# Kernel tuning notes

Measured on AMD Instinct MI355X. Metric: run time of the kernel, lower is better.

The kernel has to match this reference:

```python
import jax, jax.numpy as jnp
import numpy as np

DIM = 768

def setup_inputs() -> dict:
    key = jax.random.key(0)
    k1, k2, k3, k4, k5 = jax.random.split(key, 5)
    B, S, D = 16, 1024, DIM
    x = jax.random.normal(k1, (B, S, D), dtype=jnp.float32)
    # torch Linear weights: W has shape [out, in], y = x @ W.T + b
    w_qkv = jax.random.normal(k2, (3 * D, D), dtype=jnp.float32) * (D ** -0.5)
    b_qkv = jax.random.normal(k3, (3 * D,), dtype=jnp.float32) * 0.01
    w_out = jax.random.normal(k4, (D, D), dtype=jnp.float32) * (D ** -0.5)
    b_out = jax.random.normal(k5, (D,), dtype=jnp.float32) * 0.01
    return {"x": x, "w_qkv": w_qkv, "b_qkv": b_qkv, "w_out": w_out, "b_out": b_out}

def reference(x, w_qkv, b_qkv, w_out, b_out):
    D = x.shape[-1]
    qkv = jnp.einsum('bsd,ed->bse', x, w_qkv) + b_qkv  # [B,S,3D]
    q, k, v = jnp.split(qkv, 3, axis=-1)
    scale = D ** -0.5
    att = jnp.einsum('bqd,bkd->bqk', q, k) * scale  # [B,S,S]
    att = jax.nn.softmax(att, axis=-1)
    # dropout (p=0.1) is identity in eval mode
    out = jnp.einsum('bqk,bkd->bqd', att, v)
    return jnp.einsum('bsd,ed->bse', out, w_out) + b_out
```

## Files before the change

kernel.cpp:

```cpp
#include <hip/hip_runtime.h>
#include <hip/hip_bf16.h>
#include <math.h>

typedef __attribute__((ext_vector_type(8))) short bf16x8;
typedef __attribute__((ext_vector_type(4))) float f32x4;

__device__ __forceinline__ unsigned short f2bf_rne(float f) {
    union { float f; unsigned u; } x; x.f = f;
    unsigned r = x.u + 0x7FFFu + ((x.u >> 16) & 1u);
    return (unsigned short)(r >> 16);
}

__device__ __forceinline__ void store4(unsigned short* p, float v0, float v1, float v2, float v3) {
    ushort4 o; o.x = f2bf_rne(v0); o.y = f2bf_rne(v1); o.z = f2bf_rne(v2); o.w = f2bf_rne(v3);
    *(ushort4*)p = o;
}
__device__ __forceinline__ void store4(float* p, float v0, float v1, float v2, float v3) {
    float4 o; o.x = v0; o.y = v1; o.z = v2; o.w = v3;
    *(float4*)p = o;
}

__device__ __forceinline__ void async_copy16(const void* g, void* l) {
    __builtin_amdgcn_global_load_lds(
        (const __attribute__((address_space(1))) void*)g,
        (__attribute__((address_space(3))) void*)l, 16, 0, 0);
}

__device__ __forceinline__ void gemm_core128(
    unsigned short* shA, unsigned short* shB,
    const unsigned short* __restrict__ A, int lda,
    const unsigned short* __restrict__ B, int ldb,
    long long tileM, long long tileN, int K,
    int t, int wm, int wn, int quad, int l16, f32x4 (&acc)[4][4])
{
    for (int k0 = 0; k0 < K; k0 += 64) {
        __syncthreads();
#pragma unroll
        for (int p = 0; p < 4; ++p) {
            const int g   = p * 256 + t;
            const int row = g >> 3;
            const int kg  = (g & 7) ^ (row & 7);
            async_copy16(A + (tileM + row) * (long long)lda + k0 + kg * 8, &shA[g << 3]);
            async_copy16(B + (tileN + row) * (long long)ldb + k0 + kg * 8, &shB[g << 3]);
        }
        __syncthreads();

#pragma unroll 1
        for (int h = 0; h < 2; ++h) {
            bf16x8 af[4], bfr[4];
#pragma unroll
            for (int mi = 0; mi < 4; ++mi) {
                const int row = wm + mi * 16 + l16;
                const int kg  = ((h << 2) | quad) ^ (row & 7);
                af[mi] = *(const bf16x8*)(&shA[row * 64 + kg * 8]);
            }
#pragma unroll
            for (int ni = 0; ni < 4; ++ni) {
                const int row = wn + ni * 16 + l16;
                const int kg  = ((h << 2) | quad) ^ (row & 7);
                bfr[ni] = *(const bf16x8*)(&shB[row * 64 + kg * 8]);
            }
#pragma unroll
            for (int mi = 0; mi < 4; ++mi)
#pragma unroll
                for (int ni = 0; ni < 4; ++ni)
                    acc[mi][ni] = __builtin_amdgcn_mfma_f32_16x16x32_bf16(
                        bfr[ni], af[mi], acc[mi][ni], 0, 0, 0);
        }
    }
}

__global__ __launch_bounds__(256) void prep(
    const float* __restrict__ w_qkv, const float* __restrict__ b_qkv,
    const float* __restrict__ w_out, const float* __restrict__ b_out,
    unsigned short* __restrict__ wqT, unsigned short* __restrict__ wkT,
    unsigned short* __restrict__ wvT, unsigned short* __restrict__ wob,
    float* __restrict__ v2f, float* __restrict__ bpp)
{
    const int blk = blockIdx.x;
    const int t   = threadIdx.x;
    if (blk < 432) {
        __shared__ float sh[64][65];
        __shared__ float pv[4][64];
        const int m  = blk / 144;
        const int r  = blk % 144;
        const int ty = r / 12;
        const int tx = r % 12;
        const float* W = w_qkv + (long long)m * 768 * 768;
        unsigned short* WT = (m == 0) ? wqT : (m == 1) ? wkT : wvT;
        const int il = t & 63;
        const int ob = t >> 6;
        float acc = 0.f;
#pragma unroll
        for (int it = 0; it < 16; ++it) {
            const int ol = ob + it * 4;
            float w = W[(long long)(ty * 64 + ol) * 768 + tx * 64 + il];
            sh[ol][il] = w;
            if (m == 1) acc += w * b_qkv[ty * 64 + ol];
        }
        __syncthreads();
#pragma unroll
        for (int it = 0; it < 16; ++it) {
            const int il2 = ob + it * 4;
            WT[(long long)(tx * 64 + il2) * 768 + ty * 64 + il] = f2bf_rne(sh[il][il2]);
        }
        if (m == 1) {
            pv[ob][il] = acc;
            __syncthreads();
            if (t < 64)
                atomicAdd(&v2f[tx * 64 + t], pv[0][t] + pv[1][t] + pv[2][t] + pv[3][t]);
        }
    } else if (blk < 624) {
        const int d = (blk - 432) * 4 + (t >> 6);
        const int l = t & 63;
        float s = 0.f;
        for (int o = l; o < 768; o += 64)
            s += w_out[(long long)d * 768 + o] * b_qkv[1536 + o];
        for (int off = 1; off < 64; off <<= 1) s += __shfl_xor(s, off);
        if (l == 0) bpp[d] = b_out[d] + s;
    } else {
        const int j = (blk - 624) * 256 + t;
        float4 v = ((const float4*)w_out)[j];
        ushort4 o;
        o.x = f2bf_rne(v.x); o.y = f2bf_rne(v.y);
        o.z = f2bf_rne(v.z); o.w = f2bf_rne(v.w);
        ((ushort4*)wob)[j] = o;
    }
}

__global__ __launch_bounds__(256) void wgemm_cvt(
    const unsigned short* __restrict__ wkT, const unsigned short* __restrict__ wqT,
    const unsigned short* __restrict__ wob, const unsigned short* __restrict__ wvT,
    unsigned short* __restrict__ B2,
    const float* __restrict__ x, unsigned short* __restrict__ xb,
    const float* __restrict__ v2f, float* __restrict__ wf)
{
    const int t = threadIdx.x;
    if (blockIdx.x < 72) {
        __shared__ unsigned short shA[8192];
        __shared__ unsigned short shB[8192];
        const int lane = t & 63;
        const int wave = t >> 6;
        const int wm   = (wave & 1) * 64;
        const int wn   = (wave >> 1) * 64;
        const int quad = lane >> 4;
        const int l16  = lane & 15;
        const int z  = blockIdx.x / 36;
        const int r  = blockIdx.x % 36;
        const long long tileM = (long long)(r / 6) * 128;
        const long long tileN = (long long)(r % 6) * 128;
        const unsigned short* A  = z ? wob : wkT;
        const unsigned short* Bp = z ? wvT : wqT;
        unsigned short* C = B2 + (long long)z * 768 * 768;

        f32x4 acc[4][4];
#pragma unroll
        for (int i = 0; i < 4; ++i)
#pragma unroll
            for (int j = 0; j < 4; ++j)
#pragma unroll
                for (int rr = 0; rr < 4; ++rr) acc[i][j][rr] = 0.0f;

        gemm_core128(shA, shB, A, 768, Bp, 768, tileM, tileN, 768,
                     t, wm, wn, quad, l16, acc);

#pragma unroll
        for (int mi = 0; mi < 4; ++mi) {
            const long long gm = tileM + wm + mi * 16 + l16;
#pragma unroll
            for (int ni = 0; ni < 4; ++ni) {
                const long long gn0 = tileN + wn + ni * 16 + quad * 4;
                const f32x4 a = acc[mi][ni];
                store4(C + gm * 768 + gn0, a[0], a[1], a[2], a[3]);
            }
        }
    } else {
        const int wave = t >> 6;
        const int lane = t & 63;
        const long long row = (long long)(blockIdx.x - 72) * 4 + wave;
        const float4* xr = (const float4*)x + row * 192;
        ushort4* xbr = (ushort4*)xb + row * 192;
        const float4* v2 = (const float4*)v2f;
        float w = 0.f;
#pragma unroll
        for (int j = 0; j < 3; ++j) {
            const int c = j * 64 + lane;
            float4 v = xr[c];
            ushort4 o;
            o.x = f2bf_rne(v.x); o.y = f2bf_rne(v.y);
            o.z = f2bf_rne(v.z); o.w = f2bf_rne(v.w);
            xbr[c] = o;
            float4 b = v2[c];
            w += v.x * b.x + v.y * b.y + v.z * b.z + v.w * b.w;
        }
#pragma unroll
        for (int off = 1; off < 64; off <<= 1) w += __shfl_xor(w, off);
        if (lane == 0) wf[row] = w;
    }
}

template <typename OutT, bool DO_EXP, bool DO_RSCALE, bool DO_VT>
__global__ __launch_bounds__(256) void gemm_nt_bf16(
    const unsigned short* __restrict__ A, int lda, long long strideA,
    const unsigned short* __restrict__ B, int ldb, long long strideB,
    OutT* __restrict__ C, int ldc, long long strideC,
    const float* __restrict__ bias, float scale, int K,
    float* __restrict__ rowsum, const float* __restrict__ rscale,
    unsigned short* __restrict__ vtp, const float* __restrict__ wf)
{
    __shared__ unsigned short shA[8448];
    __shared__ unsigned short shB[8448];

    const int t    = threadIdx.x;
    const int lane = t & 63;
    const int wave = t >> 6;
    const int wm   = (wave & 1) * 64;
    const int wn   = (wave >> 1) * 64;
    const int quad = lane >> 4;
    const int l16  = lane & 15;

    const int gx = gridDim.x, gy = gridDim.y;
    const int nwg = gx * gy * gridDim.z;
    const int orig = blockIdx.x + gx * (blockIdx.y + gy * blockIdx.z);
    const int id  = (orig & 7) * (nwg >> 3) + (orig >> 3);
    const int bx  = id % gx;
    const int rem = id / gx;
    const int by  = rem % gy;
    const int bz  = rem / gy;

    const long long batch = bz;
    A += batch * strideA;
    B += batch * strideB;
    C += batch * strideC;

    const long long tileM = (long long)by * 128;
    const long long tileN = (long long)bx * 128;
    const long long rowsPerBatch = (long long)gy * 128;

    f32x4 acc[4][4];
#pragma unroll
    for (int i = 0; i < 4; ++i)
#pragma unroll
        for (int j = 0; j < 4; ++j)
#pragma unroll
            for (int r = 0; r < 4; ++r) acc[i][j][r] = 0.0f;

    gemm_core128(shA, shB, A, lda, B, ldb, tileM, tileN, K, t, wm, wn, quad, l16, acc);

    const bool vt_block = DO_VT && (tileN >= 768) && (tileN < 1536);
    if (vt_block) __syncthreads();
    unsigned short* const shd = (wn == 0) ? shA : shB;

    float wkv[4][4];
    if (DO_EXP) {
        const float* wfb = wf + batch * rowsPerBatch;
#pragma unroll
        for (int ni = 0; ni < 4; ++ni) {
            const long long gn0 = tileN + wn + ni * 16 + quad * 4;
            float4 t4 = *(const float4*)&wfb[gn0];
            wkv[ni][0] = t4.x; wkv[ni][1] = t4.y; wkv[ni][2] = t4.z; wkv[ni][3] = t4.w;
        }
    }
#pragma unroll
    for (int mi = 0; mi < 4; ++mi) {
        const long long gm = tileM + wm + mi * 16 + l16;
        float w = scale;
        if (DO_RSCALE) w = scale / rscale[batch * rowsPerBatch + gm];
        float rsum = 0.0f;
#pragma unroll
        for (int ni = 0; ni < 4; ++ni) {
            const long long gn0 = tileN + wn + ni * 16 + quad * 4;
            float b0 = 0.f, b1 = 0.f, b2 = 0.f, b3 = 0.f;
            if (bias) {
                float4 bv = *(const float4*)&bias[gn0];
                b0 = bv.x; b1 = bv.y; b2 = bv.z; b3 = bv.w;
            }
            const f32x4 a = acc[mi][ni];
            float v0, v1, v2, v3;
            if (DO_EXP) {
                v0 = __expf((a[0] + wkv[ni][0]) * scale);
                v1 = __expf((a[1] + wkv[ni][1]) * scale);
                v2 = __expf((a[2] + wkv[ni][2]) * scale);
                v3 = __expf((a[3] + wkv[ni][3]) * scale);
                rsum += (v0 + v1) + (v2 + v3);
            } else {
                v0 = a[0] * w + b0; v1 = a[1] * w + b1;
                v2 = a[2] * w + b2; v3 = a[3] * w + b3;
            }
            if (vt_block) {
                const int dl = ni * 16 + quad * 4;
                const int kl = wm + mi * 16 + l16;
                shd[(dl + 0) * 132 + kl] = f2bf_rne(v0);
                shd[(dl + 1) * 132 + kl] = f2bf_rne(v1);
                shd[(dl + 2) * 132 + kl] = f2bf_rne(v2);
                shd[(dl + 3) * 132 + kl] = f2bf_rne(v3);
            } else {
                store4(C + gm * (long long)ldc + gn0, v0, v1, v2, v3);
            }
        }
        if (DO_EXP) {
            rsum += __shfl_xor(rsum, 16);
            rsum += __shfl_xor(rsum, 32);
            if (quad == 0)
                atomicAdd(&rowsum[batch * rowsPerBatch + gm], rsum);
        }
    }
    if (vt_block) {
        __syncthreads();
        const long long bvt  = tileM >> 10;
        const long long kin0 = tileM & 1023;
        const int dr = t >> 1;
        const int hf = t & 1;
        const unsigned short* src = (dr < 64) ? &shA[dr * 132] : &shB[(dr - 64) * 132];
        unsigned short* dst = vtp + (bvt * 768 + (tileN - 768) + dr) * 1024 + kin0 + hf * 64;
        src += hf * 64;
#pragma unroll
        for (int j = 0; j < 16; ++j)
            *(uint2*)(dst + j * 4) = *(const uint2*)(src + j * 4);
    }
}

extern "C" void kernel_launch(void* const* d_in, const int* in_sizes, int n_in,
                              void* d_out, int out_size, void* d_ws, size_t ws_size,
                              hipStream_t stream) {
    (void)in_sizes; (void)n_in; (void)out_size; (void)ws_size;

    const float* x     = (const float*)d_in[0];
    const float* w_qkv = (const float*)d_in[1];
    const float* b_qkv = (const float*)d_in[2];
    const float* w_out = (const float*)d_in[3];
    const float* b_out = (const float*)d_in[4];
    float* out = (float*)d_out;

    const int B = 16, S = 1024, D = 768;
    const long long MS = (long long)B * S;
    const int NB2 = 1536;

    unsigned short* xb  = (unsigned short*)d_ws;
    unsigned short* wob = xb  + MS * D;
    unsigned short* wqT = wob + (long long)D * D;
    unsigned short* wkT = wqT + (long long)D * D;
    unsigned short* wvT = wkT + (long long)D * D;
    unsigned short* B2  = wvT + (long long)D * D;
    unsigned short* xm  = B2  + (long long)NB2 * D;
    unsigned short* vwt = xm  + MS * NB2;
    unsigned short* att = vwt + (long long)B * D * S;
    float* rsum = (float*)(att + (long long)B * S * S);
    float* v2f  = rsum + MS;
    float* bpp  = v2f + D;
    float* wf   = bpp + D;

    hipMemsetAsync(rsum, 0, (size_t)(MS + D) * sizeof(float), stream);

    prep<<<1200, 256, 0, stream>>>(w_qkv, b_qkv, w_out, b_out,
                                   wqT, wkT, wvT, wob, v2f, bpp);

    wgemm_cvt<<<4168, 256, 0, stream>>>(wkT, wqT, wob, wvT, B2, x, xb, v2f, wf);

    gemm_nt_bf16<unsigned short, false, false, true><<<dim3(NB2 / 128, (int)(MS / 128), 1), 256, 0, stream>>>(
        xb, D, 0, B2, D, 0, xm, NB2, 0, nullptr, 1.0f, D, nullptr, nullptr, vwt, nullptr);

    const float scale = 0.03608439182435162f;
    gemm_nt_bf16<unsigned short, true, false, false><<<dim3(S / 128, S / 128, B), 256, 0, stream>>>(
        xm, NB2, (long long)S * NB2,
        xb, D,   (long long)S * D,
        att, S,  (long long)S * S, nullptr, scale, D, rsum, nullptr, nullptr, wf);

    gemm_nt_bf16<float, false, true, false><<<dim3(D / 128, S / 128, B), 256, 0, stream>>>(
        att, S, (long long)S * S,
        vwt, S, (long long)D * S,
        out, D, (long long)S * D, bpp, 1.0f, S, nullptr, rsum, nullptr, nullptr);
}
```

Baseline: 259.8 us.

## Replace atomic row-sum accumulation with partial-sum slots and fold softmax scale into weights

Row sums of the exponentiated scores are now written to 16 per-column-tile partial slots instead of being accumulated with atomicAdd. The final GEMM adds those slots up, which removes the hipMemsetAsync and the atomic contention. The QK scale is folded into the precomputed Wk^T Wq product and the wf vector, so the exp epilogue loses one multiply per element. The k-bias vector is now computed in dedicated prep blocks without atomics, and xm gets a tighter stride of 768 instead of 1536. The cost is extra reads of 16 partials per row in the output GEMM.

```diff
diff --git a/kernel.cpp b/kernel.cpp
--- a/kernel.cpp
+++ b/kernel.cpp
@@ -4,6 +4,8 @@
 
 typedef __attribute__((ext_vector_type(8))) short bf16x8;
 typedef __attribute__((ext_vector_type(4))) float f32x4;
+
+#define SCALE_QK 0.03608439182435162f
 
 __device__ __forceinline__ unsigned short f2bf_rne(float f) {
     union { float f; unsigned u; } x; x.f = f;
@@ -81,7 +83,6 @@
     const int t   = threadIdx.x;
     if (blk < 432) {
         __shared__ float sh[64][65];
-        __shared__ float pv[4][64];
         const int m  = blk / 144;
         const int r  = blk % 144;
         const int ty = r / 12;
@@ -90,25 +91,16 @@
         unsigned short* WT = (m == 0) ? wqT : (m == 1) ? wkT : wvT;
         const int il = t & 63;
         const int ob = t >> 6;
-        float acc = 0.f;
 #pragma unroll
         for (int it = 0; it < 16; ++it) {
             const int ol = ob + it * 4;
-            float w = W[(long long)(ty * 64 + ol) * 768 + tx * 64 + il];
-            sh[ol][il] = w;
-            if (m == 1) acc += w * b_qkv[ty * 64 + ol];
+            sh[ol][il] = W[(long long)(ty * 64 + ol) * 768 + tx * 64 + il];
         }
         __syncthreads();
 #pragma unroll
         for (int it = 0; it < 16; ++it) {
             const int il2 = ob + it * 4;
             WT[(long long)(tx * 64 + il2) * 768 + ty * 64 + il] = f2bf_rne(sh[il][il2]);
-        }
-        if (m == 1) {
-            pv[ob][il] = acc;
-            __syncthreads();
-            if (t < 64)
-                atomicAdd(&v2f[tx * 64 + t], pv[0][t] + pv[1][t] + pv[2][t] + pv[3][t]);
         }
     } else if (blk < 624) {
         const int d = (blk - 432) * 4 + (t >> 6);
@@ -118,8 +110,20 @@
             s += w_out[(long long)d * 768 + o] * b_qkv[1536 + o];
         for (int off = 1; off < 64; off <<= 1) s += __shfl_xor(s, off);
         if (l == 0) bpp[d] = b_out[d] + s;
+    } else if (blk < 636) {
+        __shared__ float pvv[4][64];
+        const int i0   = (blk - 624) * 64;
+        const int il   = t & 63;
+        const int wave = t >> 6;
+        const float* Wk = w_qkv + 768LL * 768;
+        float a = 0.f;
+        for (int o = wave * 192; o < wave * 192 + 192; ++o)
+            a += Wk[(long long)o * 768 + i0 + il] * b_qkv[o];
+        pvv[wave][il] = a;
+        __syncthreads();
+        if (t < 64) v2f[i0 + t] = pvv[0][t] + pvv[1][t] + pvv[2][t] + pvv[3][t];
     } else {
-        const int j = (blk - 624) * 256 + t;
+        const int j = (blk - 636) * 256 + t;
         float4 v = ((const float4*)w_out)[j];
         ushort4 o;
         o.x = f2bf_rne(v.x); o.y = f2bf_rne(v.y);
@@ -152,6 +156,7 @@
         const unsigned short* A  = z ? wob : wkT;
         const unsigned short* Bp = z ? wvT : wqT;
         unsigned short* C = B2 + (long long)z * 768 * 768;
+        const float sc = z ? 1.0f : SCALE_QK;
 
         f32x4 acc[4][4];
 #pragma unroll
@@ -171,7 +176,7 @@
             for (int ni = 0; ni < 4; ++ni) {
                 const long long gn0 = tileN + wn + ni * 16 + quad * 4;
                 const f32x4 a = acc[mi][ni];
-                store4(C + gm * 768 + gn0, a[0], a[1], a[2], a[3]);
+                store4(C + gm * 768 + gn0, a[0] * sc, a[1] * sc, a[2] * sc, a[3] * sc);
             }
         }
     } else {
@@ -195,7 +200,7 @@
         }
 #pragma unroll
         for (int off = 1; off < 64; off <<= 1) w += __shfl_xor(w, off);
-        if (lane == 0) wf[row] = w;
+        if (lane == 0) wf[row] = w * SCALE_QK;
     }
 }
 
@@ -265,7 +270,13 @@
     for (int mi = 0; mi < 4; ++mi) {
         const long long gm = tileM + wm + mi * 16 + l16;
         float w = scale;
-        if (DO_RSCALE) w = scale / rscale[batch * rowsPerBatch + gm];
+        if (DO_RSCALE) {
+            float s = 0.f;
+#pragma unroll
+            for (int j = 0; j < 16; ++j)
+                s += rscale[((long long)j * gridDim.z + batch) * rowsPerBatch + gm];
+            w = scale / s;
+        }
         float rsum = 0.0f;
 #pragma unroll
         for (int ni = 0; ni < 4; ++ni) {
@@ -278,10 +289,10 @@
             const f32x4 a = acc[mi][ni];
             float v0, v1, v2, v3;
             if (DO_EXP) {
-                v0 = __expf((a[0] + wkv[ni][0]) * scale);
-                v1 = __expf((a[1] + wkv[ni][1]) * scale);
-                v2 = __expf((a[2] + wkv[ni][2]) * scale);
-                v3 = __expf((a[3] + wkv[ni][3]) * scale);
+                v0 = __expf(a[0] + wkv[ni][0]);
+                v1 = __expf(a[1] + wkv[ni][1]);
+                v2 = __expf(a[2] + wkv[ni][2]);
+                v3 = __expf(a[3] + wkv[ni][3]);
                 rsum += (v0 + v1) + (v2 + v3);
             } else {
                 v0 = a[0] * w + b0; v1 = a[1] * w + b1;
@@ -301,8 +312,10 @@
         if (DO_EXP) {
             rsum += __shfl_xor(rsum, 16);
             rsum += __shfl_xor(rsum, 32);
-            if (quad == 0)
-                atomicAdd(&rowsum[batch * rowsPerBatch + gm], rsum);
+            if (quad == 0) {
+                const long long slot = (long long)(bx * 2 + (wn >> 6));
+                rowsum[(slot * gridDim.z + batch) * rowsPerBatch + gm] = rsum;
+            }
         }
     }
     if (vt_block) {
@@ -343,31 +356,28 @@
     unsigned short* wvT = wkT + (long long)D * D;
     unsigned short* B2  = wvT + (long long)D * D;
     unsigned short* xm  = B2  + (long long)NB2 * D;
-    unsigned short* vwt = xm  + MS * NB2;
+    unsigned short* vwt = xm  + MS * D;
     unsigned short* att = vwt + (long long)B * D * S;
-    float* rsum = (float*)(att + (long long)B * S * S);
-    float* v2f  = rsum + MS;
-    float* bpp  = v2f + D;
-    float* wf   = bpp + D;
-
-    hipMemsetAsync(rsum, 0, (size_t)(MS + D) * sizeof(float), stream);
-
-    prep<<<1200, 256, 0, stream>>>(w_qkv, b_qkv, w_out, b_out,
+    float* rpart = (float*)(att + (long long)B * S * S);
+    float* v2f   = rpart + 16 * MS;
+    float* bpp   = v2f + D;
+    float* wf    = bpp + D;
+
+    prep<<<1212, 256, 0, stream>>>(w_qkv, b_qkv, w_out, b_out,
                                    wqT, wkT, wvT, wob, v2f, bpp);
 
     wgemm_cvt<<<4168, 256, 0, stream>>>(wkT, wqT, wob, wvT, B2, x, xb, v2f, wf);
 
     gemm_nt_bf16<unsigned short, false, false, true><<<dim3(NB2 / 128, (int)(MS / 128), 1), 256, 0, stream>>>(
-        xb, D, 0, B2, D, 0, xm, NB2, 0, nullptr, 1.0f, D, nullptr, nullptr, vwt, nullptr);
-
-    const float scale = 0.03608439182435162f;
+        xb, D, 0, B2, D, 0, xm, D, 0, nullptr, 1.0f, D, nullptr, nullptr, vwt, nullptr);
+
     gemm_nt_bf16<unsigned short, true, false, false><<<dim3(S / 128, S / 128, B), 256, 0, stream>>>(
-        xm, NB2, (long long)S * NB2,
-        xb, D,   (long long)S * D,
-        att, S,  (long long)S * S, nullptr, scale, D, rsum, nullptr, nullptr, wf);
+        xm, D, (long long)S * D,
+        xb, D, (long long)S * D,
+        att, S, (long long)S * S, nullptr, 1.0f, D, rpart, nullptr, nullptr, wf);
 
     gemm_nt_bf16<float, false, true, false><<<dim3(D / 128, S / 128, B), 256, 0, stream>>>(
         att, S, (long long)S * S,
         vwt, S, (long long)D * S,
-        out, D, (long long)S * D, bpp, 1.0f, S, nullptr, rsum, nullptr, nullptr);
-}
+        out, D, (long long)S * D, bpp, 1.0f, S, nullptr, rpart, nullptr, nullptr);
+}
```

Result: slower. 265.0 us (+2.0%).
